# Performance work log

Measured on AMD Instinct MI355X. Metric: run time of the kernel, lower is better.

## Reference

```python
import jax, jax.numpy as jnp
import numpy as np

EPS = 1e-8

def _address(h, w_prev, mem, Wk, bk, Wb, bb, Wg, bg, Ws, bs, Wgam, bgam):
    # h: [B,H], w_prev: [B,N], mem: [B,N,M]
    k = jnp.tanh(h @ Wk + bk)                                 # key        [B,M]
    beta = jax.nn.softplus(h @ Wb + bb)[:, None]              # strength   [B,1]
    g = jax.nn.sigmoid(h @ Wg + bg)[:, None]                  # gate       [B,1]
    s = jax.nn.softmax(h @ Ws + bs, axis=-1)                  # shift      [B,3]
    gamma = 1.0 + jax.nn.softplus(h @ Wgam + bgam)[:, None]   # sharpen    [B,1]
    # content addressing: cosine similarity
    dot = jnp.einsum('bm,bnm->bn', k, mem)                    # [B,N]
    sim = dot / (jnp.linalg.norm(k, axis=-1, keepdims=True) * jnp.linalg.norm(mem, axis=-1) + EPS)
    wc = jax.nn.softmax(beta * sim, axis=-1)
    # gated interpolation with previous weights
    wg_ = g * wc + (1.0 - g) * w_prev
    # circular convolution with 3-tap shift kernel (-1, 0, +1)
    shifted = (s[:, 0:1] * jnp.roll(wg_, 1, axis=-1)
               + s[:, 1:2] * wg_
               + s[:, 2:3] * jnp.roll(wg_, -1, axis=-1))
    # sharpening
    wp = shifted ** gamma
    return wp / (jnp.sum(wp, axis=-1, keepdims=True) + EPS)


def reference(x, mem0, wr0, ww0, h0, Wx, Wrd, bh, Wk, bk, Wb, bb, Wg, bg, Ws, bs, Wgam, bgam, We, be, Wa, ba):
    B = x.shape[0]
    mem_init = jnp.broadcast_to(mem0, (B,) + mem0.shape)  # [B,N,M]

    def step(carry, x_t):
        mem, wr, ww, h = carry
        # write to memory using previous hidden state and previous write weights
        erase = jax.nn.sigmoid(h @ We + be)               # [B,M]
        add = jnp.tanh(h @ Wa + ba)                       # [B,M]
        mem = mem * (1.0 - ww[:, :, None] * erase[:, None, :]) + ww[:, :, None] * add[:, None, :]
        # read from updated memory with previous read weights
        r = jnp.einsum('bn,bnm->bm', wr, mem)             # [B,M]
        # controller step
        h = jnp.tanh(x_t @ Wx + r @ Wrd + bh)             # [B,H]
        # update addressing weights (head 0 = read, head 1 = write)
        wr_n = _address(h, wr, mem, Wk[0], bk[0], Wb[0], bb[0], Wg[0], bg[0], Ws[0], bs[0], Wgam[0], bgam[0])
        ww_n = _address(h, ww, mem, Wk[1], bk[1], Wb[1], bb[1], Ws is None, bg[1], Ws[1], bs[1], Wgam[1], bgam[1]) if False else _address(h, ww, mem, Wk[1], bk[1], Wb[1], bb[1], Wg[1], bg[1], Ws[1], bs[1], Wgam[1], bgam[1])
        return (mem, wr_n, ww_n, h), h

    _, hids = jax.lax.scan(step, (mem_init, wr0, ww0, h0), jnp.swapaxes(x, 0, 1))
    return jnp.swapaxes(hids, 0, 1)  # [B,T,H]


def setup_inputs() -> dict:
    key = jax.random.key(0)
    B, T, D, N, M, H = 128, 128, 128, 128, 128, 256
    ks = jax.random.split(key, 16)
    sc = 0.1
    wr0 = jnp.zeros((B, N), jnp.float32).at[:, 0].set(1.0)
    return {
        'x':    jax.random.normal(ks[0], (B, T, D), jnp.float32),
        'mem0': jax.random.uniform(ks[1], (N, M), jnp.float32) * 0.1,
        'wr0':  wr0,
        'ww0':  wr0,
        'h0':   jnp.zeros((B, H), jnp.float32),
        'Wx':   jax.random.normal(ks[2], (D, H), jnp.float32) * sc,
        'Wrd':  jax.random.normal(ks[3], (M, H), jnp.float32) * sc,
        'bh':   jnp.zeros((H,), jnp.float32),
        'Wk':   jax.random.normal(ks[4], (2, H, M), jnp.float32) * sc,
        'bk':   jnp.zeros((2, M), jnp.float32),
        'Wb':   jax.random.normal(ks[5], (2, H), jnp.float32) * sc,
        'bb':   jnp.zeros((2,), jnp.float32),
        'Wg':   jax.random.normal(ks[6], (2, H), jnp.float32) * sc,
        'bg':   jnp.zeros((2,), jnp.float32),
        'Ws':   jax.random.normal(ks[7], (2, H, 3), jnp.float32) * sc,
        'bs':   jnp.zeros((2, 3), jnp.float32),
        'Wgam': jax.random.normal(ks[8], (2, H), jnp.float32) * sc,
        'bgam': jnp.zeros((2,), jnp.float32),
        'We':   jax.random.normal(ks[9], (H, M), jnp.float32) * sc,
        'be':   jnp.zeros((M,), jnp.float32),
        'Wa':   jax.random.normal(ks[10], (H, M), jnp.float32) * sc,
        'ba':   jnp.zeros((M,), jnp.float32),
    }
```

## Files before the change

### kernel.cpp

```cpp
#include <hip/hip_runtime.h>
#include <math.h>

#define Tt 128
#define NT 512
#define EPSF 1e-8f

typedef _Float16 f16x2 __attribute__((ext_vector_type(2)));

__device__ __forceinline__ float fsigmoid(float v) { return 1.f / (1.f + expf(-v)); }
__device__ __forceinline__ float fsoftplus(float v) { return (v > 20.f) ? v : log1pf(expf(v)); }
__device__ __forceinline__ float ftanh(float v) { float e = expf(2.f * v); return 1.f - 2.f / (e + 1.f); }

__device__ __forceinline__ float dot2(f16x2 a, f16x2 b, float c) {
#if __has_builtin(__builtin_amdgcn_fdot2)
  return __builtin_amdgcn_fdot2(a, b, c, false);
#else
  return c + (float)a.x * (float)b.x + (float)a.y * (float)b.y;
#endif
}
__device__ __forceinline__ f16x2 pack2(float a, float b) {
  f16x2 p; p.x = (_Float16)a; p.y = (_Float16)b; return p;
}
__device__ __forceinline__ f16x2 bc16(unsigned int v) { return __builtin_bit_cast(f16x2, v); }

template <int C> __device__ __forceinline__ float dppadd(float v) {
  int s = __builtin_amdgcn_update_dpp(0, __builtin_bit_cast(int, v), C, 0xf, 0xf, true);
  return v + __builtin_bit_cast(float, s);
}
template <int C> __device__ __forceinline__ float dppmax(float v) {
  int iv = __builtin_bit_cast(int, v);
  int s = __builtin_amdgcn_update_dpp(iv, iv, C, 0xf, 0xf, false);
  return fmaxf(v, __builtin_bit_cast(float, s));
}
__device__ __forceinline__ float qsum16(float v) {
  v = dppadd<0x111>(v); v = dppadd<0x112>(v); v = dppadd<0x114>(v); v = dppadd<0x118>(v);
  return v;
}
__device__ __forceinline__ float halfsum(float v) {
  v = qsum16(v); v = dppadd<0x142>(v);
  return v;
}
__device__ __forceinline__ float allsum(float v) {
  v = halfsum(v); v = dppadd<0x143>(v);
  return __builtin_bit_cast(float, __builtin_amdgcn_readlane(__builtin_bit_cast(int, v), 63));
}
__device__ __forceinline__ float allmax(float v) {
  v = dppmax<0x111>(v); v = dppmax<0x112>(v); v = dppmax<0x114>(v);
  v = dppmax<0x118>(v); v = dppmax<0x142>(v); v = dppmax<0x143>(v);
  return __builtin_bit_cast(float, __builtin_amdgcn_readlane(__builtin_bit_cast(int, v), 63));
}

__global__ __launch_bounds__(512, 1) void ntm_prep(
    const float* __restrict__ We, const float* __restrict__ Wa,
    const float* __restrict__ Wk, unsigned int* __restrict__ wsb)
{
  const int i = blockIdx.x * 512 + threadIdx.x;
  const int e = i & 3;
  const int cg = (i >> 2) & 63;
  const int jj4 = (i >> 8) & 3;
  const int js = (i >> 10) & 7;
  const int c = (i >> 13) & 7;
  const int jj = jj4 * 4 + e;
  const int mat = c >> 1;
  const int col = (c & 1) * 64 + cg;
  const int row0 = js * 32 + 2 * jj;
  const float* base = (mat == 0) ? We : (mat == 1) ? Wa : (mat == 2) ? Wk : (Wk + 256 * 128);
  wsb[i] = __builtin_bit_cast(unsigned int, pack2(base[row0 * 128 + col], base[(row0 + 1) * 128 + col]));
}

__global__ __launch_bounds__(NT, 1) void ntm_kernel(
    const float* __restrict__ x, const float* __restrict__ mem0,
    const float* __restrict__ wr0, const float* __restrict__ ww0,
    const float* __restrict__ h0, const float* __restrict__ Wx,
    const float* __restrict__ Wrd, const float* __restrict__ bh,
    const float* __restrict__ bk,
    const float* __restrict__ Wb, const float* __restrict__ bb,
    const float* __restrict__ Wg, const float* __restrict__ bg,
    const float* __restrict__ Ws, const float* __restrict__ bs,
    const float* __restrict__ Wgam, const float* __restrict__ bgam,
    const float* __restrict__ be, const float* __restrict__ ba,
    const uint4* __restrict__ wsb4,
    float* __restrict__ out)
{
  const int b = blockIdx.x;
  const int t = threadIdx.x;
  const int lane = t & 63;
  const int wave = t >> 6;
  const int cg = t & 63;
  const int js = t >> 6;
  const int c4 = t & 31;
  const int rs = t >> 5;

  __shared__ __align__(16) float mem[128 * 128];
  __shared__ __align__(16) uint4 lbig7[2048];
  __shared__ __align__(16) float part[4096];
  __shared__ __align__(16) float h_l[256];
  __shared__ __align__(16) float xf[128];
  __shared__ __align__(16) float rf[128];
  __shared__ __align__(16) float er[128];
  __shared__ __align__(16) float ad[128];
  __shared__ __align__(16) float kbuf[256];
  __shared__ float wsm_l[3072];
  __shared__ float wr_s[128], ww_s[128];
  __shared__ float normsq[128];
  __shared__ float dotv[256];
  __shared__ float scal[12];
  __shared__ float red2[4];
  __shared__ float bias_big[512];
  __shared__ float bh_l[256];
  __shared__ float bias_sm[12];

  f16x2 wcreg[64];
  {
    const float* basep = (js < 4) ? (Wx + (js * 32) * 256) : (Wrd + ((js - 4) * 32) * 256);
    #pragma unroll
    for (int c = 0; c < 4; ++c) {
      const float* bp = basep + c * 64 + cg;
      #pragma unroll
      for (int jj = 0; jj < 16; ++jj) {
        wcreg[c * 16 + jj] = pack2(bp[(2 * jj) * 256], bp[(2 * jj + 1) * 256]);
      }
    }
  }

  for (int i = t; i < 128 * 128; i += NT) mem[i] = mem0[i];
  for (int i = t; i < 2048; i += NT) lbig7[i] = wsb4[14336 + i];
  if (t < 128) { wr_s[t] = wr0[b * 128 + t]; ww_s[t] = ww0[b * 128 + t]; }
  if (t < 256) { h_l[t] = h0[b * 256 + t]; bh_l[t] = bh[t]; }
  bias_big[t] = (t < 128) ? be[t] : (t < 256) ? ba[t - 128] : bk[t - 256];
  for (int i = t; i < 3072; i += NT) {
    const int d = i >> 8, j = i & 255;
    const int head = d / 6, kind = d % 6;
    float v;
    if (kind == 0)      v = Wb[head * 256 + j];
    else if (kind == 1) v = Wg[head * 256 + j];
    else if (kind == 2) v = Wgam[head * 256 + j];
    else                v = Ws[head * 768 + j * 3 + (kind - 3)];
    wsm_l[i] = v;
  }
  if (t < 12) {
    const int head = t / 6, kind = t % 6;
    bias_sm[t] = (kind == 0) ? bb[head] : (kind == 1) ? bg[head]
               : (kind == 2) ? bgam[head] : bs[head * 3 + (kind - 3)];
  }
  __syncthreads();

  uint4 pf0, pf1, pf2, pf3;
  auto issue_pf = [&]() {
    const uint4* p0 = wsb4 + js * 256 + cg;
    pf0 = p0[0]; pf1 = p0[64]; pf2 = p0[128]; pf3 = p0[192];
  };

  auto phase_big4 = [&]() {
    f16x2 hh[16];
    #pragma unroll
    for (int jj = 0; jj < 16; ++jj) {
      const float2 h2 = *reinterpret_cast<const float2*>(&h_l[js * 32 + 2 * jj]);
      hh[jj] = pack2(h2.x, h2.y);
    }
    float acc[8];
    #pragma unroll
    for (int c = 0; c < 8; ++c) acc[c] = 0.f;
    #pragma unroll
    for (int c = 0; c < 8; ++c) {
      uint4 w0, w1, w2, w3;
      if (c == 0) { w0 = pf0; w1 = pf1; w2 = pf2; w3 = pf3; }
      else if (c == 7) {
        const uint4* p = lbig7 + js * 256 + cg;
        w0 = p[0]; w1 = p[64]; w2 = p[128]; w3 = p[192];
      } else {
        const uint4* p = wsb4 + (c * 8 + js) * 256 + cg;
        w0 = p[0]; w1 = p[64]; w2 = p[128]; w3 = p[192];
      }
      acc[c] = dot2(hh[0],  bc16(w0.x), acc[c]);
      acc[c] = dot2(hh[1],  bc16(w0.y), acc[c]);
      acc[c] = dot2(hh[2],  bc16(w0.z), acc[c]);
      acc[c] = dot2(hh[3],  bc16(w0.w), acc[c]);
      acc[c] = dot2(hh[4],  bc16(w1.x), acc[c]);
      acc[c] = dot2(hh[5],  bc16(w1.y), acc[c]);
      acc[c] = dot2(hh[6],  bc16(w1.z), acc[c]);
      acc[c] = dot2(hh[7],  bc16(w1.w), acc[c]);
      acc[c] = dot2(hh[8],  bc16(w2.x), acc[c]);
      acc[c] = dot2(hh[9],  bc16(w2.y), acc[c]);
      acc[c] = dot2(hh[10], bc16(w2.z), acc[c]);
      acc[c] = dot2(hh[11], bc16(w2.w), acc[c]);
      acc[c] = dot2(hh[12], bc16(w3.x), acc[c]);
      acc[c] = dot2(hh[13], bc16(w3.y), acc[c]);
      acc[c] = dot2(hh[14], bc16(w3.z), acc[c]);
      acc[c] = dot2(hh[15], bc16(w3.w), acc[c]);
    }
    #pragma unroll
    for (int c = 0; c < 8; ++c) part[js * 512 + c * 64 + cg] = acc[c];
  };

  auto phase_reduce = [&]() {
    {
      float v = bias_big[t];
      #pragma unroll
      for (int s = 0; s < 8; ++s) v += part[s * 512 + t];
      if (t < 128)      er[t] = fsigmoid(v);
      else if (t < 256) ad[t - 128] = ftanh(v);
      else {
        float kv = ftanh(v);
        kbuf[t - 256] = kv;
        float ks = kv * kv;
        ks = halfsum(ks); ks = dppadd<0x143>(ks);
        if (lane == 63) red2[wave - 4] = ks;
      }
    }
    if (t < 384) {
      const int d = t >> 5, l5 = t & 31;
      float s = 0.f;
      #pragma unroll
      for (int q = 0; q < 8; ++q) s += h_l[l5 + 32 * q] * wsm_l[d * 256 + l5 + 32 * q];
      s = halfsum(s);
      if ((lane & 31) == 31) scal[d] = s + bias_sm[d];
    }
  };

  issue_pf();
  phase_big4();
  __syncthreads();
  phase_reduce();
  __syncthreads();

  for (int step = 0; step < Tt; ++step) {
    issue_pf();

    if (t < 128) xf[t] = x[((size_t)b * Tt + step) * 128 + t];
    {
      const float4 e4 = *reinterpret_cast<const float4*>(&er[c4 * 4]);
      const float4 a4 = *reinterpret_cast<const float4*>(&ad[c4 * 4]);
      float rx = 0.f, ry = 0.f, rz = 0.f, rw = 0.f;
      #pragma unroll
      for (int k = 0; k < 8; ++k) {
        const int n = rs + 16 * k;
        const float wwn = ww_s[n], wrn = wr_s[n];
        float4 v = *reinterpret_cast<const float4*>(&mem[n * 128 + c4 * 4]);
        v.x = v.x * (1.f - wwn * e4.x) + wwn * a4.x;
        v.y = v.y * (1.f - wwn * e4.y) + wwn * a4.y;
        v.z = v.z * (1.f - wwn * e4.z) + wwn * a4.z;
        v.w = v.w * (1.f - wwn * e4.w) + wwn * a4.w;
        *reinterpret_cast<float4*>(&mem[n * 128 + c4 * 4]) = v;
        rx += wrn * v.x; ry += wrn * v.y; rz += wrn * v.z; rw += wrn * v.w;
      }
      *reinterpret_cast<float4*>(&part[rs * 128 + c4 * 4]) = make_float4(rx, ry, rz, rw);
    }
    __syncthreads();

    if (t < 128) {
      float r = 0.f;
      #pragma unroll
      for (int s = 0; s < 16; ++s) r += part[s * 128 + t];
      rf[t] = r;
    }
    __syncthreads();

    {
      const float* src = (js < 4) ? (xf + js * 32) : (rf + (js - 4) * 32);
      float acc[4];
      #pragma unroll
      for (int c = 0; c < 4; ++c) acc[c] = 0.f;
      #pragma unroll
      for (int jj = 0; jj < 16; ++jj) {
        const float2 s2 = *reinterpret_cast<const float2*>(&src[2 * jj]);
        const f16x2 xx = pack2(s2.x, s2.y);
        #pragma unroll
        for (int c = 0; c < 4; ++c) acc[c] = dot2(xx, wcreg[c * 16 + jj], acc[c]);
      }
      #pragma unroll
      for (int c = 0; c < 4; ++c) part[js * 256 + c * 64 + cg] = acc[c];
    }
    __syncthreads();

    if (t < 256) {
      float v = bh_l[t];
      #pragma unroll
      for (int s = 0; s < 8; ++s) v += part[s * 256 + t];
      v = ftanh(v);
      h_l[t] = v;
      out[((size_t)b * Tt + step) * 256 + t] = v;
    }
    __syncthreads();

    phase_big4();
    __syncthreads();
    phase_reduce();
    __syncthreads();

    {
      const int head = t >> 8;
      const int u = t & 255;
      const int cc = u & 31, ns = u >> 5;
      const float4 k4 = *reinterpret_cast<const float4*>(&kbuf[head * 128 + cc * 4]);
      #pragma unroll
      for (int ch = 0; ch < 2; ++ch) {
        float dsum[8], qsum[8];
        #pragma unroll
        for (int ii = 0; ii < 8; ++ii) {
          const int n = ns * 16 + ch * 8 + ii;
          const float4 m4 = *reinterpret_cast<const float4*>(&mem[n * 128 + cc * 4]);
          dsum[ii] = k4.x * m4.x + k4.y * m4.y + k4.z * m4.z + k4.w * m4.w;
          qsum[ii] = m4.x * m4.x + m4.y * m4.y + m4.z * m4.z + m4.w * m4.w;
        }
        #pragma unroll
        for (int ii = 0; ii < 8; ++ii) dsum[ii] = halfsum(dsum[ii]);
        if (head == 0) {
          #pragma unroll
          for (int ii = 0; ii < 8; ++ii) qsum[ii] = halfsum(qsum[ii]);
        }
        if ((lane & 31) == 31) {
          #pragma unroll
          for (int ii = 0; ii < 8; ++ii) dotv[head * 128 + ns * 16 + ch * 8 + ii] = dsum[ii];
          if (head == 0) {
            #pragma unroll
            for (int ii = 0; ii < 8; ++ii) normsq[ns * 16 + ch * 8 + ii] = qsum[ii];
          }
        }
      }
    }
    __syncthreads();

    if (wave < 2) {
      const int head = wave;
      const int h6 = head * 6;
      const float beta  = fsoftplus(scal[h6]);
      const float g     = fsigmoid(scal[h6 + 1]);
      const float gamma = 1.f + fsoftplus(scal[h6 + 2]);
      float e0 = scal[h6 + 3], e1 = scal[h6 + 4], e2 = scal[h6 + 5];
      const float mx3 = fmaxf(e0, fmaxf(e1, e2));
      float x0 = expf(e0 - mx3), x1 = expf(e1 - mx3), x2 = expf(e2 - mx3);
      const float si = 1.f / (x0 + x1 + x2);
      const float s0 = x0 * si, s1 = x1 * si, s2 = x2 * si;
      const float knorm = sqrtf(red2[2 * head] + red2[2 * head + 1]);
      float* wprev = head ? ww_s : wr_s;
      const int n0 = 2 * lane, n1 = 2 * lane + 1;
      float l0 = beta * dotv[head * 128 + n0] / (knorm * sqrtf(normsq[n0]) + EPSF);
      float l1 = beta * dotv[head * 128 + n1] / (knorm * sqrtf(normsq[n1]) + EPSF);
      const float mx = allmax(fmaxf(l0, l1));
      float q0 = expf(l0 - mx), q1 = expf(l1 - mx);
      const float inv = 1.f / allsum(q0 + q1);
      const float wg0 = g * q0 * inv + (1.f - g) * wprev[n0];
      const float wg1 = g * q1 * inv + (1.f - g) * wprev[n1];
      const float wgl = __shfl(wg1, (lane + 63) & 63);
      const float wgr = __shfl(wg0, (lane + 1) & 63);
      const float sh0 = s0 * wgl + s1 * wg0 + s2 * wg1;
      const float sh1 = s0 * wg0 + s1 * wg1 + s2 * wgr;
      const float wp0 = exp2f(gamma * log2f(sh0));
      const float wp1 = exp2f(gamma * log2f(sh1));
      const float itot = 1.f / (allsum(wp0 + wp1) + EPSF);
      wprev[n0] = wp0 * itot;
      wprev[n1] = wp1 * itot;
    }
    __syncthreads();
  }
}

extern "C" void kernel_launch(void* const* d_in, const int* in_sizes, int n_in,
                              void* d_out, int out_size, void* d_ws, size_t ws_size,
                              hipStream_t stream) {
  const float* x    = (const float*)d_in[0];
  const float* mem0 = (const float*)d_in[1];
  const float* wr0  = (const float*)d_in[2];
  const float* ww0  = (const float*)d_in[3];
  const float* h0   = (const float*)d_in[4];
  const float* Wx   = (const float*)d_in[5];
  const float* Wrd  = (const float*)d_in[6];
  const float* bh   = (const float*)d_in[7];
  const float* Wk   = (const float*)d_in[8];
  const float* bk   = (const float*)d_in[9];
  const float* Wb   = (const float*)d_in[10];
  const float* bb   = (const float*)d_in[11];
  const float* Wg   = (const float*)d_in[12];
  const float* bg   = (const float*)d_in[13];
  const float* Ws   = (const float*)d_in[14];
  const float* bs   = (const float*)d_in[15];
  const float* Wgam = (const float*)d_in[16];
  const float* bgam = (const float*)d_in[17];
  const float* We   = (const float*)d_in[18];
  const float* be   = (const float*)d_in[19];
  const float* Wa   = (const float*)d_in[20];
  const float* ba   = (const float*)d_in[21];
  float* out = (float*)d_out;
  unsigned int* wsb = (unsigned int*)d_ws;

  hipLaunchKernelGGL(ntm_prep, dim3(128), dim3(512), 0, stream, We, Wa, Wk, wsb);
  hipLaunchKernelGGL(ntm_kernel, dim3(128), dim3(NT), 0, stream,
                     x, mem0, wr0, ww0, h0, Wx, Wrd, bh, bk, Wb, bb,
                     Wg, bg, Ws, bs, Wgam, bgam, be, ba,
                     (const uint4*)wsb, out);
}
```

Baseline: 834.3 us.

## Give each thread a full output column in the big GEMV, removing the partial reduction

Repacks the big fused weight matrix (erase/add/key projections) so each thread owns one output column across all 256 inputs. It reads the packed fp16 hidden state from shared memory as a broadcast. This removes the cross-slice partial-sum buffer, the separate reduction phase and one block barrier per step. A larger share of the weights (7 of 32 chunks instead of 1 of 8) now sits in LDS. The tradeoff is a longer serial dot chain per thread, four accumulators instead of eight independent ones, and more LDS used for cached weights.

Measured after the change: 801.4 us. 3.9% less time.

```diff
diff --git a/kernel.cpp b/kernel.cpp
--- a/kernel.cpp
+++ b/kernel.cpp
@@ -56,16 +56,14 @@
 {
   const int i = blockIdx.x * 512 + threadIdx.x;
   const int e = i & 3;
-  const int cg = (i >> 2) & 63;
-  const int jj4 = (i >> 8) & 3;
-  const int js = (i >> 10) & 7;
-  const int c = (i >> 13) & 7;
-  const int jj = jj4 * 4 + e;
-  const int mat = c >> 1;
-  const int col = (c & 1) * 64 + cg;
-  const int row0 = js * 32 + 2 * jj;
+  const int col = (i >> 2) & 511;
+  const int q = i >> 11;
+  const int k0 = 8 * q + 2 * e;
+  const int mat = col >> 7;
+  const int mcol = col & 127;
   const float* base = (mat == 0) ? We : (mat == 1) ? Wa : (mat == 2) ? Wk : (Wk + 256 * 128);
-  wsb[i] = __builtin_bit_cast(unsigned int, pack2(base[row0 * 128 + col], base[(row0 + 1) * 128 + col]));
+  wsb[i] = __builtin_bit_cast(unsigned int,
+             pack2(base[k0 * 128 + mcol], base[(k0 + 1) * 128 + mcol]));
 }
 
 __global__ __launch_bounds__(NT, 1) void ntm_kernel(
@@ -92,9 +90,10 @@
   const int rs = t >> 5;
 
   __shared__ __align__(16) float mem[128 * 128];
-  __shared__ __align__(16) uint4 lbig7[2048];
-  __shared__ __align__(16) float part[4096];
+  __shared__ __align__(16) uint4 lbigq[3584];
+  __shared__ __align__(16) float part[2048];
   __shared__ __align__(16) float h_l[256];
+  __shared__ __align__(16) unsigned int h16[128];
   __shared__ __align__(16) float xf[128];
   __shared__ __align__(16) float rf[128];
   __shared__ __align__(16) float er[128];
@@ -124,9 +123,14 @@
   }
 
   for (int i = t; i < 128 * 128; i += NT) mem[i] = mem0[i];
-  for (int i = t; i < 2048; i += NT) lbig7[i] = wsb4[14336 + i];
+  for (int i = t; i < 3584; i += NT) lbigq[i] = wsb4[12800 + i];
   if (t < 128) { wr_s[t] = wr0[b * 128 + t]; ww_s[t] = ww0[b * 128 + t]; }
-  if (t < 256) { h_l[t] = h0[b * 256 + t]; bh_l[t] = bh[t]; }
+  if (t < 256) {
+    float v = h0[b * 256 + t];
+    h_l[t] = v; bh_l[t] = bh[t];
+    const float vo = __shfl_xor(v, 1);
+    if (!(t & 1)) h16[t >> 1] = __builtin_bit_cast(unsigned int, pack2(v, vo));
+  }
   bias_big[t] = (t < 128) ? be[t] : (t < 256) ? ba[t - 128] : bk[t - 256];
   for (int i = t; i < 3072; i += NT) {
     const int d = i >> 8, j = i & 255;
@@ -145,68 +149,37 @@
   }
   __syncthreads();
 
-  uint4 pf0, pf1, pf2, pf3;
+  const uint4* h16_4 = reinterpret_cast<const uint4*>(h16);
+
+  uint4 pf[4];
   auto issue_pf = [&]() {
-    const uint4* p0 = wsb4 + js * 256 + cg;
-    pf0 = p0[0]; pf1 = p0[64]; pf2 = p0[128]; pf3 = p0[192];
+    #pragma unroll
+    for (int q = 0; q < 4; ++q) pf[q] = wsb4[q * 512 + t];
   };
 
   auto phase_big4 = [&]() {
-    f16x2 hh[16];
+    float a0 = 0.f, a1 = 0.f, a2 = 0.f, a3 = 0.f;
     #pragma unroll
-    for (int jj = 0; jj < 16; ++jj) {
-      const float2 h2 = *reinterpret_cast<const float2*>(&h_l[js * 32 + 2 * jj]);
-      hh[jj] = pack2(h2.x, h2.y);
-    }
-    float acc[8];
-    #pragma unroll
-    for (int c = 0; c < 8; ++c) acc[c] = 0.f;
-    #pragma unroll
-    for (int c = 0; c < 8; ++c) {
-      uint4 w0, w1, w2, w3;
-      if (c == 0) { w0 = pf0; w1 = pf1; w2 = pf2; w3 = pf3; }
-      else if (c == 7) {
-        const uint4* p = lbig7 + js * 256 + cg;
-        w0 = p[0]; w1 = p[64]; w2 = p[128]; w3 = p[192];
-      } else {
-        const uint4* p = wsb4 + (c * 8 + js) * 256 + cg;
-        w0 = p[0]; w1 = p[64]; w2 = p[128]; w3 = p[192];
-      }
-      acc[c] = dot2(hh[0],  bc16(w0.x), acc[c]);
-      acc[c] = dot2(hh[1],  bc16(w0.y), acc[c]);
-      acc[c] = dot2(hh[2],  bc16(w0.z), acc[c]);
-      acc[c] = dot2(hh[3],  bc16(w0.w), acc[c]);
-      acc[c] = dot2(hh[4],  bc16(w1.x), acc[c]);
-      acc[c] = dot2(hh[5],  bc16(w1.y), acc[c]);
-      acc[c] = dot2(hh[6],  bc16(w1.z), acc[c]);
-      acc[c] = dot2(hh[7],  bc16(w1.w), acc[c]);
-      acc[c] = dot2(hh[8],  bc16(w2.x), acc[c]);
-      acc[c] = dot2(hh[9],  bc16(w2.y), acc[c]);
-      acc[c] = dot2(hh[10], bc16(w2.z), acc[c]);
-      acc[c] = dot2(hh[11], bc16(w2.w), acc[c]);
-      acc[c] = dot2(hh[12], bc16(w3.x), acc[c]);
-      acc[c] = dot2(hh[13], bc16(w3.y), acc[c]);
-      acc[c] = dot2(hh[14], bc16(w3.z), acc[c]);
-      acc[c] = dot2(hh[15], bc16(w3.w), acc[c]);
-    }
-    #pragma unroll
-    for (int c = 0; c < 8; ++c) part[js * 512 + c * 64 + cg] = acc[c];
-  };
-
-  auto phase_reduce = [&]() {
-    {
-      float v = bias_big[t];
-      #pragma unroll
-      for (int s = 0; s < 8; ++s) v += part[s * 512 + t];
-      if (t < 128)      er[t] = fsigmoid(v);
-      else if (t < 256) ad[t - 128] = ftanh(v);
-      else {
-        float kv = ftanh(v);
-        kbuf[t - 256] = kv;
-        float ks = kv * kv;
-        ks = halfsum(ks); ks = dppadd<0x143>(ks);
-        if (lane == 63) red2[wave - 4] = ks;
-      }
+    for (int q = 0; q < 32; ++q) {
+      uint4 w;
+      if (q < 4)        w = pf[q];
+      else if (q >= 25) w = lbigq[(q - 25) * 512 + t];
+      else              w = wsb4[q * 512 + t];
+      const uint4 hq = h16_4[q];
+      a0 = dot2(bc16(hq.x), bc16(w.x), a0);
+      a1 = dot2(bc16(hq.y), bc16(w.y), a1);
+      a2 = dot2(bc16(hq.z), bc16(w.z), a2);
+      a3 = dot2(bc16(hq.w), bc16(w.w), a3);
+    }
+    const float acc = (a0 + a1) + (a2 + a3) + bias_big[t];
+    if (t < 128)      er[t] = fsigmoid(acc);
+    else if (t < 256) ad[t - 128] = ftanh(acc);
+    else {
+      const float kv = ftanh(acc);
+      kbuf[t - 256] = kv;
+      float ks = kv * kv;
+      ks = halfsum(ks); ks = dppadd<0x143>(ks);
+      if (lane == 63) red2[wave - 4] = ks;
     }
     if (t < 384) {
       const int d = t >> 5, l5 = t & 31;
@@ -220,8 +193,6 @@
 
   issue_pf();
   phase_big4();
-  __syncthreads();
-  phase_reduce();
   __syncthreads();
 
   for (int step = 0; step < Tt; ++step) {
@@ -280,12 +251,12 @@
       v = ftanh(v);
       h_l[t] = v;
       out[((size_t)b * Tt + step) * 256 + t] = v;
+      const float vo = __shfl_xor(v, 1);
+      if (!(t & 1)) h16[t >> 1] = __builtin_bit_cast(unsigned int, pack2(v, vo));
     }
     __syncthreads();
 
     phase_big4();
-    __syncthreads();
-    phase_reduce();
     __syncthreads();
 
     {
```
